# Kernel tuning notes

Hardware: AMD Instinct MI355X
Metric: run time of the kernel (lower is better)

## Reference

```python
import jax, jax.numpy as jnp
import numpy as np

N_NODES = 100000
NEG_SLOPE = 0.2


def gat_conv(x, edge_src, edge_dst, W, att_src, att_dst, bias):
    """PyG-style GATConv with heads=1. edge_src/edge_dst include self-loops.
    x: [N, F_in], W: [F_in, F_out], att_src/att_dst: [F_out], bias: [F_out].
    """
    n = x.shape[0]
    h = x @ W  # [N, F_out]
    a_src = h @ att_src  # [N]
    a_dst = h @ att_dst  # [N]
    e = jax.nn.leaky_relu(a_src[edge_src] + a_dst[edge_dst], NEG_SLOPE)  # [E]
    # segment softmax over edges sharing a destination node
    m = jax.ops.segment_max(e, edge_dst, num_segments=n)  # [N]; self-loops ensure no empty segment
    p = jnp.exp(e - m[edge_dst])
    denom = jax.ops.segment_sum(p, edge_dst, num_segments=n)  # [N]
    alpha = p / denom[edge_dst]  # [E]
    out = jax.ops.segment_sum(alpha[:, None] * h[edge_src], edge_dst, num_segments=n)
    return out + bias


def setup_inputs() -> dict:
    key = jax.random.key(0)
    ks = jax.random.split(key, 16)
    n, e = N_NODES, 1_600_000
    f_in, f_hid, f_out = 128, 64, 32
    x = jax.random.normal(ks[0], (n, f_in), dtype=jnp.float32)
    edge_index = jax.random.randint(ks[1], (2, e), 0, n, dtype=jnp.int32)

    def lin(k, fi, fo):
        return jax.random.normal(k, (fi, fo), dtype=jnp.float32) / np.sqrt(fi).astype(np.float32)

    def att(k, fo):
        return jax.random.normal(k, (fo,), dtype=jnp.float32) / np.sqrt(fo).astype(np.float32)

    return {
        "x": x, "edge_index": edge_index,
        "W1": lin(ks[2], f_in, f_hid), "as1": att(ks[3], f_hid), "ad1": att(ks[4], f_hid),
        "b1": jnp.zeros((f_hid,), jnp.float32),
        "W2": lin(ks[5], f_hid, f_hid), "as2": att(ks[6], f_hid), "ad2": att(ks[7], f_hid),
        "b2": jnp.zeros((f_hid,), jnp.float32),
        "W3": lin(ks[8], f_hid, f_out), "as3": att(ks[9], f_out), "ad3": att(ks[10], f_out),
        "b3": jnp.zeros((f_out,), jnp.float32),
    }


def reference(x, edge_index, W1, as1, ad1, b1, W2, as2, ad2, b2, W3, as3, ad3, b3):
    n = x.shape[0]
    # PyG GATConv default add_self_loops=True
    loops = jnp.arange(n, dtype=edge_index.dtype)
    src = jnp.concatenate([edge_index[0], loops])
    dst = jnp.concatenate([edge_index[1], loops])

    h1 = jax.nn.relu(gat_conv(x, src, dst, W1, as1, ad1, b1))
    h2 = jax.nn.relu(gat_conv(h1, src, dst, W2, as2, ad2, b2))
    out = gat_conv(h2, src, dst, W3, as3, ad3, b3)
    return (out, h1, h2)
```

## Files before the change

kernel.cpp:

```cpp
#include <hip/hip_runtime.h>
#include <hip/hip_bf16.h>

#define NEG_SLOPE 0.2f

__device__ __forceinline__ unsigned short bf16bits(float f) {
    __hip_bfloat16 t = __float2bfloat16(f);
    return *reinterpret_cast<unsigned short*>(&t);
}

template <int FIN, int FOUT>
__global__ __launch_bounds__(256) void node_linear(
    const float* __restrict__ x, const float* __restrict__ W,
    const float* __restrict__ att_s, const float* __restrict__ att_d,
    __hip_bfloat16* __restrict__ h, float* __restrict__ a_s, float* __restrict__ a_d, int n)
{
    constexpr int FG = FOUT / 4;
    constexpr int NG = 256 / FG;
    constexpr int NB = NG * 4;
    constexpr int RS = FIN + 4;
    __shared__ float xs[NB * RS];

    const int tid = threadIdx.x;
    const int base = blockIdx.x * NB;

    constexpr int CNT = NB * FIN / 4 / 256;
    #pragma unroll
    for (int i = 0; i < CNT; ++i) {
        int f4 = tid + 256 * i;
        int node = f4 / (FIN / 4);
        int kk = f4 % (FIN / 4);
        float4 v = make_float4(0.f, 0.f, 0.f, 0.f);
        if (base + node < n) v = *(const float4*)(x + (size_t)(base + node) * FIN + kk * 4);
        *(float4*)(xs + node * RS + kk * 4) = v;
    }
    __syncthreads();

    const int fg = tid % FG;
    const int ng = tid / FG;
    const float* wp = W + fg * 4;
    const float* xr0 = xs + (ng * 4 + 0) * RS;
    const float* xr1 = xs + (ng * 4 + 1) * RS;
    const float* xr2 = xs + (ng * 4 + 2) * RS;
    const float* xr3 = xs + (ng * 4 + 3) * RS;

    float a00=0,a01=0,a02=0,a03=0, a10=0,a11=0,a12=0,a13=0;
    float a20=0,a21=0,a22=0,a23=0, a30=0,a31=0,a32=0,a33=0;
    #pragma unroll 4
    for (int k = 0; k < FIN; ++k) {
        float4 w = *(const float4*)(wp + (size_t)k * FOUT);
        float x0 = xr0[k], x1 = xr1[k], x2 = xr2[k], x3 = xr3[k];
        a00 = fmaf(x0, w.x, a00); a01 = fmaf(x0, w.y, a01);
        a02 = fmaf(x0, w.z, a02); a03 = fmaf(x0, w.w, a03);
        a10 = fmaf(x1, w.x, a10); a11 = fmaf(x1, w.y, a11);
        a12 = fmaf(x1, w.z, a12); a13 = fmaf(x1, w.w, a13);
        a20 = fmaf(x2, w.x, a20); a21 = fmaf(x2, w.y, a21);
        a22 = fmaf(x2, w.z, a22); a23 = fmaf(x2, w.w, a23);
        a30 = fmaf(x3, w.x, a30); a31 = fmaf(x3, w.y, a31);
        a32 = fmaf(x3, w.z, a32); a33 = fmaf(x3, w.w, a33);
    }

    const float4 ats = *(const float4*)(att_s + fg * 4);
    const float4 atd = *(const float4*)(att_d + fg * 4);
    float acc[4][4] = {{a00,a01,a02,a03},{a10,a11,a12,a13},
                       {a20,a21,a22,a23},{a30,a31,a32,a33}};
    #pragma unroll
    for (int i = 0; i < 4; ++i) {
        int node = base + ng * 4 + i;
        float ps = acc[i][0]*ats.x + acc[i][1]*ats.y + acc[i][2]*ats.z + acc[i][3]*ats.w;
        float pd = acc[i][0]*atd.x + acc[i][1]*atd.y + acc[i][2]*atd.z + acc[i][3]*atd.w;
        #pragma unroll
        for (int o = FG / 2; o > 0; o >>= 1) {
            ps += __shfl_xor(ps, o);
            pd += __shfl_xor(pd, o);
        }
        if (fg == 0 && node < n) { a_s[node] = ps; a_d[node] = pd; }
        if (node < n) {
            unsigned w0 = (unsigned)bf16bits(acc[i][0]) | ((unsigned)bf16bits(acc[i][1]) << 16);
            unsigned w1 = (unsigned)bf16bits(acc[i][2]) | ((unsigned)bf16bits(acc[i][3]) << 16);
            uint2 pk; pk.x = w0; pk.y = w1;
            *reinterpret_cast<uint2*>(h + (size_t)node * FOUT + fg * 4) = pk;
        }
    }
}


__global__ __launch_bounds__(256) void sb_hist(
    const int* __restrict__ edst, int E, int n, int* __restrict__ sbhist)
{
    __shared__ int lh[256];
    const int tid = threadIdx.x;
    lh[tid] = 0;
    __syncthreads();
    const int Etot = E + n;
    const int stride = gridDim.x * 256;
    for (int i = blockIdx.x * 256 + tid; i < Etot; i += stride) {
        int d = (i < E) ? edst[i] : i - E;
        atomicAdd(&lh[d >> 9], 1);
    }
    __syncthreads();
    if (lh[tid] > 0) atomicAdd(&sbhist[tid], lh[tid]);
}

__global__ __launch_bounds__(256) void sb_scan(
    const int* __restrict__ sbhist, int nsb, int Etot,
    int* __restrict__ sbbase, int* __restrict__ sbcur)
{
    __shared__ int buf[256];
    const int tid = threadIdx.x;
    int v = (tid < nsb) ? sbhist[tid] : 0;
    buf[tid] = v;
    __syncthreads();
    for (int off = 1; off < 256; off <<= 1) {
        int t = (tid >= off) ? buf[tid - off] : 0;
        __syncthreads();
        buf[tid] += t;
        __syncthreads();
    }
    if (tid < nsb) {
        int ex = buf[tid] - v;
        sbbase[tid] = ex;
        sbcur[tid] = ex;
    }
    if (tid == 0) sbbase[nsb] = Etot;
}

#define CB_CHUNK 4096
#define CB_NSB_MAX 256
__global__ __launch_bounds__(256) void chunk_bin(
    const int* __restrict__ esrc, const int* __restrict__ edst, int E, int n,
    int nsb, int* __restrict__ sbcur, int* __restrict__ packed1)
{
    __shared__ int pk[CB_CHUNK];
    __shared__ unsigned short sbv[CB_CHUNK];
    __shared__ int hist[CB_NSB_MAX];
    __shared__ int gbase[CB_NSB_MAX];
    const int tid = threadIdx.x;
    const int i0 = blockIdx.x * CB_CHUNK;
    const int Etot = E + n;

    hist[tid] = 0;
    __syncthreads();

    for (int j = tid; j < CB_CHUNK; j += 256) {
        int i = i0 + j;
        if (i < Etot) {
            int s, d;
            if (i < E) { s = esrc[i]; d = edst[i]; }
            else       { s = d = i - E; }
            int sb = d >> 9;
            pk[j] = ((d & 511) << 17) | s;
            sbv[j] = (unsigned short)sb;
            atomicAdd(&hist[sb], 1);
        } else {
            sbv[j] = 0xFFFFu;
        }
    }
    __syncthreads();

    if (tid < nsb && hist[tid] > 0)
        gbase[tid] = atomicAdd(&sbcur[tid], hist[tid]);
    hist[tid] = 0;
    __syncthreads();

    for (int j = tid; j < CB_CHUNK; j += 256) {
        unsigned short sb = sbv[j];
        if (sb != 0xFFFFu) {
            int pos = gbase[sb] + atomicAdd(&hist[sb], 1);
            packed1[pos] = pk[j];
        }
    }
}

__global__ __launch_bounds__(256) void sb_sort2(
    const int* __restrict__ sbbase, const int* __restrict__ packed1,
    int* __restrict__ col, int* __restrict__ row_end, int n)
{
    const int sb = blockIdx.x;
    const int node0 = sb << 9;
    const int lo = sbbase[sb];
    const int hi = sbbase[sb + 1];
    const int tid = threadIdx.x;
    __shared__ int c[512];
    __shared__ int sc[512];
    c[tid] = 0; c[tid + 256] = 0;
    __syncthreads();
    for (int j = lo + tid; j < hi; j += 256)
        atomicAdd(&c[((unsigned)packed1[j]) >> 17], 1);
    __syncthreads();
    sc[tid] = c[tid]; sc[tid + 256] = c[tid + 256];
    __syncthreads();
    for (int off = 1; off < 512; off <<= 1) {
        int i0 = tid, i1 = tid + 256;
        int v0 = (i0 >= off) ? sc[i0 - off] : 0;
        int v1 = (i1 >= off) ? sc[i1 - off] : 0;
        __syncthreads();
        sc[i0] += v0; sc[i1] += v1;
        __syncthreads();
    }
    #pragma unroll
    for (int q = 0; q < 2; ++q) {
        int i = tid + q * 256;
        int node = node0 + i;
        if (node < n) row_end[node] = lo + sc[i];
        c[i] = lo + sc[i] - c[i];
    }
    __syncthreads();
    for (int j = lo + tid; j < hi; j += 256) {
        int p = packed1[j];
        int ld = ((unsigned)p) >> 17;
        int pos = atomicAdd(&c[ld], 1);
        col[pos] = p & 0x1FFFF;
    }
}

template <int FOUT>
__global__ __launch_bounds__(256) void gat_aggregate(
    const int* __restrict__ row_end, const int* __restrict__ col,
    const float* __restrict__ a_s, const float* __restrict__ a_d,
    const __hip_bfloat16* __restrict__ h_, const float* __restrict__ bias,
    float* __restrict__ outp, int n, int do_relu)
{
    constexpr int LPN = FOUT / 4;
    constexpr int NPW = 64 / LPN;
    const unsigned short* h = (const unsigned short*)h_;
    const int gwave = (blockIdx.x * 256 + threadIdx.x) >> 6;
    const int lane = threadIdx.x & 63;
    const int node = gwave * NPW + lane / LPN;
    const int lsub = lane % LPN;
    if (node >= n) return;
    const int end = row_end[node];
    const int start = (node == 0) ? 0 : row_end[node - 1];
    const float adn = a_d[node];
    const int egrp = lane & ~(LPN - 1);
    float acc0 = 0.f, acc1 = 0.f, acc2 = 0.f, acc3 = 0.f, den = 0.f;
    for (int j = start; j < end; j += LPN) {
        int kmax = end - j; if (kmax > LPN) kmax = LPN;
        int k_idx = j + lsub;
        int sown = col[(k_idx < end) ? k_idx : (end - 1)];
        float eown = a_s[sown] + adn;
        eown = (eown > 0.f) ? eown : NEG_SLOPE * eown;
        float pown = (lsub < kmax) ? __expf(eown) : 0.f;
        for (int k = 0; k < kmax; ++k) {
            int   sk = __shfl(sown, egrp + k);
            float pk = __shfl(pown, egrp + k);
            den += pk;
            uint2 hv = *(const uint2*)(h + (size_t)sk * FOUT + lsub * 4);
            acc0 = fmaf(pk, __uint_as_float(hv.x << 16), acc0);
            acc1 = fmaf(pk, __uint_as_float(hv.x & 0xFFFF0000u), acc1);
            acc2 = fmaf(pk, __uint_as_float(hv.y << 16), acc2);
            acc3 = fmaf(pk, __uint_as_float(hv.y & 0xFFFF0000u), acc3);
        }
    }
    const float4 b4 = *(const float4*)(bias + lsub * 4);
    float inv = 1.f / den;
    float v0 = acc0 * inv + b4.x;
    float v1 = acc1 * inv + b4.y;
    float v2 = acc2 * inv + b4.z;
    float v3 = acc3 * inv + b4.w;
    if (do_relu) {
        v0 = fmaxf(v0, 0.f); v1 = fmaxf(v1, 0.f);
        v2 = fmaxf(v2, 0.f); v3 = fmaxf(v3, 0.f);
    }
    float4 o; o.x = v0; o.y = v1; o.z = v2; o.w = v3;
    *(float4*)(outp + (size_t)node * FOUT + lsub * 4) = o;
}

extern "C" void kernel_launch(void* const* d_in, const int* in_sizes, int n_in,
                              void* d_out, int out_size, void* d_ws, size_t ws_size,
                              hipStream_t stream)
{
    const float* x   = (const float*)d_in[0];
    const int* eidx  = (const int*)d_in[1];
    const float* W1  = (const float*)d_in[2];
    const float* as1 = (const float*)d_in[3];
    const float* ad1 = (const float*)d_in[4];
    const float* b1  = (const float*)d_in[5];
    const float* W2  = (const float*)d_in[6];
    const float* as2 = (const float*)d_in[7];
    const float* ad2 = (const float*)d_in[8];
    const float* b2  = (const float*)d_in[9];
    const float* W3  = (const float*)d_in[10];
    const float* as3 = (const float*)d_in[11];
    const float* ad3 = (const float*)d_in[12];
    const float* b3  = (const float*)d_in[13];

    const int fhid = in_sizes[3];
    const int fin  = in_sizes[2] / fhid;
    const int fo3  = in_sizes[11];
    const int n    = in_sizes[0] / fin;
    const int E    = in_sizes[1] / 2;
    const int Etot = E + n;
    const int nsb  = (n + 511) >> 9;

    const int* esrc = eidx;
    const int* edst = eidx + E;

    float* out = (float*)d_out;
    float* h1  = out + (size_t)n * fo3;
    float* h2  = h1 + (size_t)n * fhid;

    int* sbhist   = (int*)d_ws;
    int* sbbase   = sbhist + 256;
    int* sbcur    = sbbase + 260;
    int* row_end  = sbcur + 256;
    int* packed1  = row_end + n;
    int* col      = packed1 + Etot;
    __hip_bfloat16* h = (__hip_bfloat16*)(col + Etot);
    float* a_s    = (float*)(h + (size_t)n * fhid);
    float* a_d    = a_s + n;

    const int nchunks = (Etot + CB_CHUNK - 1) / CB_CHUNK;

    hipMemsetAsync(sbhist, 0, 256 * 4, stream);
    sb_hist<<<1024, 256, 0, stream>>>(edst, E, n, sbhist);
    sb_scan<<<1, 256, 0, stream>>>(sbhist, nsb, Etot, sbbase, sbcur);
    chunk_bin<<<nchunks, 256, 0, stream>>>(esrc, edst, E, n, nsb, sbcur, packed1);
    sb_sort2<<<nsb, 256, 0, stream>>>(sbbase, packed1, col, row_end, n);

    const int NLB64  = (n + 63) / 64;
    const int NLB128 = (n + 127) / 128;
    const int AGG64 = (n + 3) / 4;
    const int AGG32 = (n + 7) / 8;

    node_linear<128, 64><<<NLB64, 256, 0, stream>>>(x, W1, as1, ad1, h, a_s, a_d, n);
    gat_aggregate<64><<<(n + 15) / 16, 256, 0, stream>>>(row_end, col, a_s, a_d, h, b1, h1, n, 1);

    node_linear<64, 64><<<NLB64, 256, 0, stream>>>(h1, W2, as2, ad2, h, a_s, a_d, n);
    gat_aggregate<64><<<(n + 15) / 16, 256, 0, stream>>>(row_end, col, a_s, a_d, h, b2, h2, n, 1);

    node_linear<64, 32><<<NLB128, 256, 0, stream>>>(h2, W3, as3, ad3, h, a_s, a_d, n);
    gat_aggregate<32><<<(n + 31) / 32, 256, 0, stream>>>(row_end, col, a_s, a_d, h, b3, out, n, 0);
}
```

Baseline: 323.6 us.

## Compute node linear transform with bf16 MFMA instead of scalar FMA

Rewrites the per-layer node_linear kernel to stage x and a transposed W tile in shared memory as bf16 and compute h with 16x16x32 bf16 MFMA instructions, 64 nodes per block. Attention scores a_s/a_d are accumulated from the MFMA outputs and reduced with lane shuffles. This cuts FP32 FMA work, but inputs are rounded to bf16 before the matmul, which lowers precision. The per-block W transpose and the scalar bf16 stores of h add overhead.

After: 292.6 us. 9.6% less time.

```diff
diff --git a/kernel.cpp b/kernel.cpp
--- a/kernel.cpp
+++ b/kernel.cpp
@@ -2,6 +2,9 @@
 #include <hip/hip_bf16.h>
 
 #define NEG_SLOPE 0.2f
+
+typedef __attribute__((ext_vector_type(8))) short bf16x8;
+typedef __attribute__((ext_vector_type(4))) float f32x4;
 
 __device__ __forceinline__ unsigned short bf16bits(float f) {
     __hip_bfloat16 t = __float2bfloat16(f);
@@ -14,72 +17,58 @@
     const float* __restrict__ att_s, const float* __restrict__ att_d,
     __hip_bfloat16* __restrict__ h, float* __restrict__ a_s, float* __restrict__ a_d, int n)
 {
-    constexpr int FG = FOUT / 4;
-    constexpr int NG = 256 / FG;
-    constexpr int NB = NG * 4;
-    constexpr int RS = FIN + 4;
-    __shared__ float xs[NB * RS];
-
-    const int tid = threadIdx.x;
-    const int base = blockIdx.x * NB;
-
-    constexpr int CNT = NB * FIN / 4 / 256;
+    constexpr int RS = FIN + 8;
+    __shared__ unsigned short xt[64 * RS];
+    __shared__ unsigned short Wt[FOUT * RS];
+    const int tid = threadIdx.x;
+    const int base = blockIdx.x * 64;
+
+    for (int i = tid; i < 64 * FIN / 2; i += 256) {
+        int node = i / (FIN / 2);
+        int k2 = i % (FIN / 2);
+        float2 v = make_float2(0.f, 0.f);
+        if (base + node < n) v = *(const float2*)(x + (size_t)(base + node) * FIN + k2 * 2);
+        unsigned pk = (unsigned)bf16bits(v.x) | ((unsigned)bf16bits(v.y) << 16);
+        *(unsigned*)(&xt[node * RS + k2 * 2]) = pk;
+    }
+    for (int i = tid; i < FIN * FOUT; i += 256) {
+        int k = i / FOUT, f = i % FOUT;
+        Wt[f * RS + k] = bf16bits(W[i]);
+    }
+    __syncthreads();
+
+    const int wv = tid >> 6, lane = tid & 63;
+    const int m = lane & 15, b = lane >> 4;
+    const int node0 = base + wv * 16;
+
+    float ps[4] = {0,0,0,0}, pd[4] = {0,0,0,0};
     #pragma unroll
-    for (int i = 0; i < CNT; ++i) {
-        int f4 = tid + 256 * i;
-        int node = f4 / (FIN / 4);
-        int kk = f4 % (FIN / 4);
-        float4 v = make_float4(0.f, 0.f, 0.f, 0.f);
-        if (base + node < n) v = *(const float4*)(x + (size_t)(base + node) * FIN + kk * 4);
-        *(float4*)(xs + node * RS + kk * 4) = v;
-    }
-    __syncthreads();
-
-    const int fg = tid % FG;
-    const int ng = tid / FG;
-    const float* wp = W + fg * 4;
-    const float* xr0 = xs + (ng * 4 + 0) * RS;
-    const float* xr1 = xs + (ng * 4 + 1) * RS;
-    const float* xr2 = xs + (ng * 4 + 2) * RS;
-    const float* xr3 = xs + (ng * 4 + 3) * RS;
-
-    float a00=0,a01=0,a02=0,a03=0, a10=0,a11=0,a12=0,a13=0;
-    float a20=0,a21=0,a22=0,a23=0, a30=0,a31=0,a32=0,a33=0;
-    #pragma unroll 4
-    for (int k = 0; k < FIN; ++k) {
-        float4 w = *(const float4*)(wp + (size_t)k * FOUT);
-        float x0 = xr0[k], x1 = xr1[k], x2 = xr2[k], x3 = xr3[k];
-        a00 = fmaf(x0, w.x, a00); a01 = fmaf(x0, w.y, a01);
-        a02 = fmaf(x0, w.z, a02); a03 = fmaf(x0, w.w, a03);
-        a10 = fmaf(x1, w.x, a10); a11 = fmaf(x1, w.y, a11);
-        a12 = fmaf(x1, w.z, a12); a13 = fmaf(x1, w.w, a13);
-        a20 = fmaf(x2, w.x, a20); a21 = fmaf(x2, w.y, a21);
-        a22 = fmaf(x2, w.z, a22); a23 = fmaf(x2, w.w, a23);
-        a30 = fmaf(x3, w.x, a30); a31 = fmaf(x3, w.y, a31);
-        a32 = fmaf(x3, w.z, a32); a33 = fmaf(x3, w.w, a33);
-    }
-
-    const float4 ats = *(const float4*)(att_s + fg * 4);
-    const float4 atd = *(const float4*)(att_d + fg * 4);
-    float acc[4][4] = {{a00,a01,a02,a03},{a10,a11,a12,a13},
-                       {a20,a21,a22,a23},{a30,a31,a32,a33}};
+    for (int t = 0; t < FOUT / 16; ++t) {
+        f32x4 acc = {0.f, 0.f, 0.f, 0.f};
+        #pragma unroll
+        for (int ks = 0; ks < FIN / 32; ++ks) {
+            bf16x8 a  = *(const bf16x8*)(&xt[(wv * 16 + m) * RS + ks * 32 + b * 8]);
+            bf16x8 bb = *(const bf16x8*)(&Wt[(t * 16 + m) * RS + ks * 32 + b * 8]);
+            acc = __builtin_amdgcn_mfma_f32_16x16x32_bf16(a, bb, acc, 0, 0, 0);
+        }
+        const float as_c = att_s[t * 16 + m];
+        const float ad_c = att_d[t * 16 + m];
+        #pragma unroll
+        for (int r = 0; r < 4; ++r) {
+            float v = acc[r];
+            int node = node0 + b * 4 + r;
+            if (node < n) h[(size_t)node * FOUT + t * 16 + m] = __float2bfloat16(v);
+            ps[r] = fmaf(v, as_c, ps[r]);
+            pd[r] = fmaf(v, ad_c, pd[r]);
+        }
+    }
     #pragma unroll
-    for (int i = 0; i < 4; ++i) {
-        int node = base + ng * 4 + i;
-        float ps = acc[i][0]*ats.x + acc[i][1]*ats.y + acc[i][2]*ats.z + acc[i][3]*ats.w;
-        float pd = acc[i][0]*atd.x + acc[i][1]*atd.y + acc[i][2]*atd.z + acc[i][3]*atd.w;
+    for (int r = 0; r < 4; ++r) {
+        float s = ps[r], d = pd[r];
         #pragma unroll
-        for (int o = FG / 2; o > 0; o >>= 1) {
-            ps += __shfl_xor(ps, o);
-            pd += __shfl_xor(pd, o);
-        }
-        if (fg == 0 && node < n) { a_s[node] = ps; a_d[node] = pd; }
-        if (node < n) {
-            unsigned w0 = (unsigned)bf16bits(acc[i][0]) | ((unsigned)bf16bits(acc[i][1]) << 16);
-            unsigned w1 = (unsigned)bf16bits(acc[i][2]) | ((unsigned)bf16bits(acc[i][3]) << 16);
-            uint2 pk; pk.x = w0; pk.y = w1;
-            *reinterpret_cast<uint2*>(h + (size_t)node * FOUT + fg * 4) = pk;
-        }
+        for (int o = 8; o > 0; o >>= 1) { s += __shfl_xor(s, o); d += __shfl_xor(d, o); }
+        int node = node0 + b * 4 + r;
+        if (m == 0 && node < n) { a_s[node] = s; a_d[node] = d; }
     }
 }
 
@@ -317,17 +306,14 @@
     chunk_bin<<<nchunks, 256, 0, stream>>>(esrc, edst, E, n, nsb, sbcur, packed1);
     sb_sort2<<<nsb, 256, 0, stream>>>(sbbase, packed1, col, row_end, n);
 
-    const int NLB64  = (n + 63) / 64;
-    const int NLB128 = (n + 127) / 128;
-    const int AGG64 = (n + 3) / 4;
-    const int AGG32 = (n + 7) / 8;
-
-    node_linear<128, 64><<<NLB64, 256, 0, stream>>>(x, W1, as1, ad1, h, a_s, a_d, n);
+    const int NLB = (n + 63) / 64;
+
+    node_linear<128, 64><<<NLB, 256, 0, stream>>>(x, W1, as1, ad1, h, a_s, a_d, n);
     gat_aggregate<64><<<(n + 15) / 16, 256, 0, stream>>>(row_end, col, a_s, a_d, h, b1, h1, n, 1);
 
-    node_linear<64, 64><<<NLB64, 256, 0, stream>>>(h1, W2, as2, ad2, h, a_s, a_d, n);
+    node_linear<64, 64><<<NLB, 256, 0, stream>>>(h1, W2, as2, ad2, h, a_s, a_d, n);
     gat_aggregate<64><<<(n + 15) / 16, 256, 0, stream>>>(row_end, col, a_s, a_d, h, b2, h2, n, 1);
 
-    node_linear<64, 32><<<NLB128, 256, 0, stream>>>(h2, W3, as3, ad3, h, a_s, a_d, n);
+    node_linear<64, 32><<<NLB, 256, 0, stream>>>(h2, W3, as3, ad3, h, a_s, a_d, n);
     gat_aggregate<32><<<(n + 31) / 32, 256, 0, stream>>>(row_end, col, a_s, a_d, h, b3, out, n, 0);
 }
```
